# Kernel tuning notes

Hardware: AMD Instinct MI355X
Metric: run time of the kernel (lower is better)

The kernel has to match this reference:

```python
import jax, jax.numpy as jnp
import numpy as np

ALPHA = 0.25
GAMMA = 2.0
# all cost weights are 1.0 per init defaults

def box_cxcywh_to_xyxy(b):
    cx, cy, w, h = b[..., 0], b[..., 1], b[..., 2], b[..., 3]
    return jnp.stack([cx - 0.5 * w, cy - 0.5 * h, cx + 0.5 * w, cy + 0.5 * h], axis=-1)

def generalized_box_iou(b1, b2):
    # b1: [B,Q,4], b2: [B,T,4] in xyxy -> [B,Q,T]
    area1 = (b1[..., 2] - b1[..., 0]) * (b1[..., 3] - b1[..., 1])  # [B,Q]
    area2 = (b2[..., 2] - b2[..., 0]) * (b2[..., 3] - b2[..., 1])  # [B,T]
    lt = jnp.maximum(b1[:, :, None, :2], b2[:, None, :, :2])        # [B,Q,T,2]
    rb = jnp.minimum(b1[:, :, None, 2:], b2[:, None, :, 2:])
    wh = jnp.clip(rb - lt, 0.0)
    inter = wh[..., 0] * wh[..., 1]
    union = area1[:, :, None] + area2[:, None, :] - inter
    iou = inter / union
    lt_c = jnp.minimum(b1[:, :, None, :2], b2[:, None, :, :2])
    rb_c = jnp.maximum(b1[:, :, None, 2:], b2[:, None, :, 2:])
    wh_c = jnp.clip(rb_c - lt_c, 0.0)
    area_c = wh_c[..., 0] * wh_c[..., 1]
    return iou - (area_c - union) / area_c

def point_sample_bilinear(img, pts):
    # img: [B,N,H,W]; pts: [P,2] (x,y) in [0,1]. Matches F.grid_sample
    # bilinear, align_corners=False, padding_mode='zeros'.
    H, W = img.shape[-2], img.shape[-1]
    x = pts[:, 0] * W - 0.5
    y = pts[:, 1] * H - 0.5
    x0 = jnp.floor(x); y0 = jnp.floor(y)
    wx1 = x - x0; wx0 = 1.0 - wx1
    wy1 = y - y0; wy0 = 1.0 - wy1

    def gather(yi, xi):
        valid = ((xi >= 0) & (xi < W) & (yi >= 0) & (yi < H)).astype(img.dtype)
        xc = jnp.clip(xi, 0, W - 1).astype(jnp.int32)
        yc = jnp.clip(yi, 0, H - 1).astype(jnp.int32)
        return img[:, :, yc, xc] * valid  # [B,N,P]

    return (gather(y0, x0) * (wy0 * wx0)
            + gather(y0, x0 + 1) * (wy0 * wx1)
            + gather(y0 + 1, x0) * (wy1 * wx0)
            + gather(y0 + 1, x0 + 1) * (wy1 * wx1))

def point_sample_nearest(img, pts):
    # grid_sample nearest, align_corners=False, zeros padding
    H, W = img.shape[-2], img.shape[-1]
    x = jnp.round(pts[:, 0] * W - 0.5)
    y = jnp.round(pts[:, 1] * H - 0.5)
    valid = ((x >= 0) & (x < W) & (y >= 0) & (y < H)).astype(img.dtype)
    xc = jnp.clip(x, 0, W - 1).astype(jnp.int32)
    yc = jnp.clip(y, 0, H - 1).astype(jnp.int32)
    return img[:, :, yc, xc] * valid  # [B,N,P]

def setup_inputs() -> dict:
    key = jax.random.key(0)
    ks = jax.random.split(key, 7)
    B, Q, C, T, H, W = 2, 900, 91, 64, 128, 128
    P = H * W // 16  # mask_point_sample_ratio = 16
    return {
        "pred_logits": jax.random.normal(ks[0], (B, Q, C), jnp.float32),
        "pred_boxes": jax.random.uniform(ks[1], (B, Q, 4), jnp.float32),
        "pred_masks": jax.random.normal(ks[2], (B, Q, H, W), jnp.float32),
        "tgt_boxes": jax.random.uniform(ks[3], (B, T, 4), jnp.float32),
        "tgt_masks": jax.random.uniform(ks[4], (B, T, H, W), jnp.float32),
        "point_coords": jax.random.uniform(ks[5], (1, P, 2), jnp.float32),
        "tgt_labels": jax.random.randint(ks[6], (B, T), 0, C, jnp.int32),
    }

def reference(pred_logits, pred_boxes, pred_masks, tgt_boxes, tgt_masks, point_coords, tgt_labels):
    # ---- focal classification cost ----
    prob = jax.nn.sigmoid(pred_logits)                          # [B,Q,C]
    neg_cost = (1 - ALPHA) * prob ** GAMMA * (-jax.nn.log_sigmoid(-pred_logits))
    pos_cost = ALPHA * (1 - prob) ** GAMMA * (-jax.nn.log_sigmoid(pred_logits))
    diff = pos_cost - neg_cost                                   # [B,Q,C]
    cost_class = jnp.take_along_axis(diff, tgt_labels[:, None, :], axis=2)  # [B,Q,T]

    # ---- L1 bbox cost (cdist p=1) ----
    cost_bbox = jnp.abs(pred_boxes[:, :, None, :] - tgt_boxes[:, None, :, :]).sum(-1)

    # ---- GIoU cost ----
    giou = generalized_box_iou(box_cxcywh_to_xyxy(pred_boxes), box_cxcywh_to_xyxy(tgt_boxes))

    # ---- point-sampled mask CE / Dice costs ----
    pts = point_coords[0]                                        # [P,2]
    P = pts.shape[0]
    pred_pts = point_sample_bilinear(pred_masks, pts)            # [B,Q,P]
    tgt_pts = point_sample_nearest(tgt_masks, pts)               # [B,T,P]
    pos_ce = -jax.nn.log_sigmoid(pred_pts)
    neg_ce = -jax.nn.log_sigmoid(-pred_pts)
    cost_ce = (jnp.einsum('bqp,btp->bqt', pos_ce, tgt_pts)
               + jnp.einsum('bqp,btp->bqt', neg_ce, 1.0 - tgt_pts)) / P
    s = jax.nn.sigmoid(pred_pts)
    numer = 2.0 * jnp.einsum('bqp,btp->bqt', s, tgt_pts)
    denom = s.sum(-1)[:, :, None] + tgt_pts.sum(-1)[:, None, :]
    cost_dice = 1.0 - (numer + 1.0) / (denom + 1.0)

    C = (cost_bbox + cost_class - giou + cost_ce + cost_dice).astype(jnp.float32)
    # replace non-finite entries by 2 * (per-batch max finite cost)
    fin = jnp.isfinite(C)
    max_cost = jnp.max(jnp.where(fin, C, 0.0), axis=(1, 2), keepdims=True)
    C = jnp.where(fin, C, 2.0 * max_cost)
    return C
```

## Files before the change

kernel.cpp:

```cpp
#include <hip/hip_runtime.h>
#include <hip/hip_bf16.h>
#include <math.h>

#define B_    2
#define Q_    900
#define QPAD_ 912
#define MT_   57
#define CC_   91
#define T_    64
#define H_    128
#define W_    128
#define HW_   (H_*W_)
#define P_    1024
#define FLT_BIG 3.402823466e+38f

typedef short short8 __attribute__((ext_vector_type(8)));
typedef float f32x4  __attribute__((ext_vector_type(4)));

static __device__ __forceinline__ unsigned short f2bf(float v) {
    __hip_bfloat16 h = __float2bfloat16(v);
    return *reinterpret_cast<unsigned short*>(&h);
}

__global__ __launch_bounds__(256) void kS_sample(
    const float* __restrict__ tgt_masks,
    const float* __restrict__ pred_masks,
    const float* __restrict__ pc,
    unsigned short* __restrict__ tgtPT,
    float* __restrict__ tsum,
    unsigned short* __restrict__ xsbuf,
    float* __restrict__ lneg,
    float* __restrict__ lsum,
    float* __restrict__ bmax)
{
    const int tid = threadIdx.x;
    const int wv = tid >> 6, lane = tid & 63;
    __shared__ float sSum[2][4];

    if (blockIdx.x < B_*T_) {
        if (blockIdx.x == 0 && tid < B_) bmax[tid] = 0.f;
        const int bt = blockIdx.x;
        const float* __restrict__ img = tgt_masks + (size_t)bt * HW_;

        float vals[4];
        #pragma unroll
        for (int k = 0; k < 4; ++k) {
            int p = tid*4 + k;
            float px = pc[2*p], py = pc[2*p+1];
            float xf = rintf(px * (float)W_ - 0.5f);
            float yf = rintf(py * (float)H_ - 0.5f);
            bool nv = (xf >= 0.f) && (xf < (float)W_) && (yf >= 0.f) && (yf < (float)H_);
            int xc = (int)fminf(fmaxf(xf, 0.f), (float)(W_-1));
            int yc = (int)fminf(fmaxf(yf, 0.f), (float)(H_-1));
            vals[k] = nv ? img[yc*W_ + xc] : 0.f;
        }
        *(ushort4*)(tgtPT + (size_t)bt*P_ + tid*4) =
            make_ushort4(f2bf(vals[0]), f2bf(vals[1]), f2bf(vals[2]), f2bf(vals[3]));

        float local = (vals[0] + vals[1]) + (vals[2] + vals[3]);
        #pragma unroll
        for (int off = 32; off; off >>= 1) local += __shfl_down(local, off);
        if (lane == 0) sSum[0][wv] = local;
        __syncthreads();
        if (tid == 0) tsum[bt] = (sSum[0][0]+sSum[0][1]) + (sSum[0][2]+sSum[0][3]);
    } else {
        const int bq = blockIdx.x - B_*T_;
        const int b = bq / Q_, q = bq % Q_;
        const float* __restrict__ img = pred_masks + (size_t)bq * HW_;

        int   base0[4], base1[4];
        float wp0[4], wp1[4], wyv0[4], wyv1[4];
        #pragma unroll
        for (int k = 0; k < 4; ++k) {
            int p = tid*4 + k;
            float px = pc[2*p], py = pc[2*p+1];
            float xf = px * (float)W_ - 0.5f;
            float yf = py * (float)H_ - 0.5f;
            float x0f = floorf(xf), y0f = floorf(yf);
            float wx1 = xf - x0f, wx0 = 1.f - wx1;
            float wy1 = yf - y0f, wy0 = 1.f - wy1;
            int x0 = (int)x0f, y0 = (int)y0f;
            int xa = min(max(x0, 0), W_-2);
            wp0[k] = (x0 == xa) ? wx0 : ((x0 < xa) ? wx1 : 0.f);
            wp1[k] = (x0 == xa) ? wx1 : ((x0 > xa) ? wx0 : 0.f);
            wyv0[k] = (y0 >= 0 && y0 < H_)       ? wy0 : 0.f;
            wyv1[k] = (y0+1 >= 0 && y0+1 < H_)   ? wy1 : 0.f;
            int ya0 = min(max(y0,   0), H_-1);
            int ya1 = min(max(y0+1, 0), H_-1);
            base0[k] = ya0*W_ + xa;
            base1[k] = ya1*W_ + xa;
        }

        float2 r0[4], r1[4];
        #pragma unroll
        for (int k = 0; k < 4; ++k) {
            __builtin_memcpy(&r0[k], img + base0[k], 8);
            __builtin_memcpy(&r1[k], img + base1[k], 8);
        }

        float ln = 0.f, ls = 0.f;
        unsigned short px_[4], ps_[4];
        #pragma unroll
        for (int k = 0; k < 4; ++k) {
            float x = wyv0[k]*(wp0[k]*r0[k].x + wp1[k]*r0[k].y)
                    + wyv1[k]*(wp0[k]*r1[k].x + wp1[k]*r1[k].y);
            float e  = __expf(-fabsf(x));
            float sp = __logf(1.f + e) + fmaxf(x, 0.f);
            float rr = 1.f / (1.f + e);
            float s  = (x >= 0.f) ? rr : e * rr;
            ln += sp; ls += s;
            px_[k] = f2bf(x); ps_[k] = f2bf(s);
        }

        *(ushort4*)(xsbuf + ((size_t)(b*2+0)*QPAD_ + q)*P_ + tid*4) = make_ushort4(px_[0],px_[1],px_[2],px_[3]);
        *(ushort4*)(xsbuf + ((size_t)(b*2+1)*QPAD_ + q)*P_ + tid*4) = make_ushort4(ps_[0],ps_[1],ps_[2],ps_[3]);

        #pragma unroll
        for (int off = 32; off; off >>= 1) {
            ln += __shfl_down(ln, off);
            ls += __shfl_down(ls, off);
        }
        if (lane == 0) { sSum[0][wv] = ln; sSum[1][wv] = ls; }
        __syncthreads();
        if (tid == 0) {
            lneg[b*Q_ + q] = (sSum[0][0]+sSum[0][1]) + (sSum[0][2]+sSum[0][3]);
            lsum[b*Q_ + q] = (sSum[1][0]+sSum[1][1]) + (sSum[1][2]+sSum[1][3]);
        }
    }
}

__global__ __launch_bounds__(256) void k3_gemm(
    const unsigned short* __restrict__ xsbuf,
    const unsigned short* __restrict__ tgtPT,
    const float* __restrict__ lneg,
    const float* __restrict__ lsum,
    const float* __restrict__ tsum,
    const float* __restrict__ pred_logits,
    const float* __restrict__ pred_boxes,
    const float* __restrict__ tgt_boxes,
    const int*   __restrict__ tgt_labels,
    float* __restrict__ out,
    float* __restrict__ bmax)
{
    __shared__ float sT[2][4][4][65];

    const int bid = blockIdx.x;
    const int b = bid / (MT_*4);
    const int rem = bid % (MT_*4);
    const int mt = rem >> 2, nt = rem & 3;
    const int w = threadIdx.x >> 6, l = threadIdx.x & 63;
    const int ml = l & 15, kg = l >> 4;

    const short* Ax = (const short*)xsbuf + ((size_t)(b*2+0)*QPAD_ + mt*16 + ml)*P_ + kg*8 + w*256;
    const short* As = (const short*)xsbuf + ((size_t)(b*2+1)*QPAD_ + mt*16 + ml)*P_ + kg*8 + w*256;
    const short* Bb = (const short*)tgtPT + ((size_t)(b*T_) + nt*16 + ml)*P_ + kg*8 + w*256;

    f32x4 accX = {0,0,0,0};
    f32x4 accS = {0,0,0,0};

    #pragma unroll
    for (int kt = 0; kt < 8; ++kt) {
        const int ko = kt * 32;
        short8 afx = *(const short8*)(Ax + ko);
        short8 afs = *(const short8*)(As + ko);
        short8 bf  = *(const short8*)(Bb + ko);
        accX = __builtin_amdgcn_mfma_f32_16x16x32_bf16(afx, bf, accX, 0, 0, 0);
        accS = __builtin_amdgcn_mfma_f32_16x16x32_bf16(afs, bf, accS, 0, 0, 0);
    }

    #pragma unroll
    for (int r = 0; r < 4; ++r) {
        sT[0][r][w][l] = accX[r];
        sT[1][r][w][l] = accS[r];
    }
    __syncthreads();

    const int tid = threadIdx.x;
    const int ql = tid >> 4, tc = tid & 15;
    const int r   = ql & 3;
    const int src = (ql >> 2)*16 + tc;

    float aX = ((sT[0][r][0][src] + sT[0][r][1][src]) + (sT[0][r][2][src] + sT[0][r][3][src]));
    float aS = ((sT[1][r][0][src] + sT[1][r][1][src]) + (sT[1][r][2][src] + sT[1][r][3][src]));

    const int q = mt*16 + ql;
    const int t = nt*16 + tc;
    const int qc = min(q, Q_-1);

    const float tsu = tsum[b*T_ + t];
    const int   lab = tgt_labels[b*T_ + t];
    const float4 tbx = *(const float4*)(tgt_boxes + (size_t)(b*T_ + t)*4);
    float ln  = lneg[b*Q_ + qc];
    float lsv = lsum[b*Q_ + qc];
    float4 pb = *(const float4*)(pred_boxes + (size_t)(b*Q_ + qc)*4);
    float lg  = pred_logits[((size_t)(b*Q_ + qc))*CC_ + lab];

    float ce   = (ln - aX) * (1.f/(float)P_);
    float dice = 1.f - (2.f*aS + 1.f) / (lsv + tsu + 1.f);

    float e  = __expf(-fabsf(lg));
    float lp = log1pf(e);
    float sp_neg = lp + fmaxf(-lg, 0.f);
    float sp_pos = lp + fmaxf( lg, 0.f);
    float prob = 1.f / (1.f + __expf(-lg));
    float cclass = 0.25f*(1.f-prob)*(1.f-prob)*sp_neg - 0.75f*prob*prob*sp_pos;

    float cbbox = fabsf(pb.x-tbx.x) + fabsf(pb.y-tbx.y) + fabsf(pb.z-tbx.z) + fabsf(pb.w-tbx.w);
    float px1 = pb.x - 0.5f*pb.z, py1 = pb.y - 0.5f*pb.w;
    float px2 = pb.x + 0.5f*pb.z, py2 = pb.y + 0.5f*pb.w;
    float tx1 = tbx.x - 0.5f*tbx.z, ty1 = tbx.y - 0.5f*tbx.w;
    float tx2 = tbx.x + 0.5f*tbx.z, ty2 = tbx.y + 0.5f*tbx.w;
    float a1 = (px2-px1)*(py2-py1);
    float a2 = (tx2-tx1)*(ty2-ty1);
    float iw = fmaxf(fminf(px2,tx2) - fmaxf(px1,tx1), 0.f);
    float ih = fmaxf(fminf(py2,ty2) - fmaxf(py1,ty1), 0.f);
    float inter = iw*ih;
    float uni = a1 + a2 - inter;
    float iou = inter / uni;
    float cw = fmaxf(fmaxf(px2,tx2) - fminf(px1,tx1), 0.f);
    float ch = fmaxf(fmaxf(py2,ty2) - fminf(py1,ty1), 0.f);
    float ac = cw*ch;
    float giou = iou - (ac - uni)/ac;

    float cost = cbbox + cclass - giou + ce + dice;
    float mloc = 0.f;
    if (q < Q_) {
        out[((size_t)(b*Q_ + q))*T_ + t] = cost;
        mloc = (fabsf(cost) <= FLT_BIG) ? fmaxf(cost, 0.f) : 0.f;
    }

    #pragma unroll
    for (int off = 32; off; off >>= 1) mloc = fmaxf(mloc, __shfl_down(mloc, off));
    __shared__ float sm[4];
    if (l == 0) sm[w] = mloc;
    __syncthreads();
    if (tid == 0) {
        float bm = fmaxf(fmaxf(sm[0], sm[1]), fmaxf(sm[2], sm[3]));
        atomicMax((unsigned int*)&bmax[b], __float_as_uint(bm));
    }
}

__global__ __launch_bounds__(256) void k5_fix(float* __restrict__ out,
                                              const float* __restrict__ bmax)
{
    int i = blockIdx.x*256 + threadIdx.x;
    if (i >= B_*Q_*T_) return;
    float v = out[i];
    if (!(fabsf(v) <= FLT_BIG))
        out[i] = 2.f * bmax[i / (Q_*T_)];
}

extern "C" void kernel_launch(void* const* d_in, const int* in_sizes, int n_in,
                              void* d_out, int out_size, void* d_ws, size_t ws_size,
                              hipStream_t stream) {
    const float* pred_logits  = (const float*)d_in[0];
    const float* pred_boxes   = (const float*)d_in[1];
    const float* pred_masks   = (const float*)d_in[2];
    const float* tgt_boxes    = (const float*)d_in[3];
    const float* tgt_masks    = (const float*)d_in[4];
    const float* point_coords = (const float*)d_in[5];
    const int*   tgt_labels   = (const int*)d_in[6];
    float* out = (float*)d_out;

    char* w = (char*)d_ws;
    unsigned short* tgtPT = (unsigned short*)w;
    unsigned short* xsbuf = (unsigned short*)(w + 262144);
    size_t xs_bytes = (size_t)B_*2*QPAD_*P_*2;
    char* w2 = w + 262144 + xs_bytes;
    float* tsum = (float*)w2;
    float* lneg = (float*)(w2 + 512);
    float* lsum = (float*)(w2 + 512 + 7296);
    float* bmax = (float*)(w2 + 512 + 2*7296);

    kS_sample<<<B_*T_ + B_*Q_, 256, 0, stream>>>(tgt_masks, pred_masks, point_coords,
                                                 tgtPT, tsum, xsbuf, lneg, lsum, bmax);
    k3_gemm<<<B_*MT_*4, 256, 0, stream>>>(xsbuf, tgtPT, lneg, lsum, tsum,
                                          pred_logits, pred_boxes, tgt_boxes, tgt_labels, out, bmax);
    k5_fix<<<(B_*Q_*T_ + 255)/256, 256, 0, stream>>>(out, bmax);
}
```

Measured before the change: 47.63 us.

## Stage full mask images into LDS via async global_load_lds before point sampling

Each sampling block copies its entire 128x128 mask into shared memory with direct global-to-LDS loads, then performs the nearest and bilinear gathers from LDS. This replaces scattered global gathers with coalesced bulk loads. It uses 64 KB of LDS per block, which limits occupancy, and it reads every pixel even where only sampled pixels are needed.

```diff
diff --git a/kernel.cpp b/kernel.cpp
--- a/kernel.cpp
+++ b/kernel.cpp
@@ -14,6 +14,9 @@
 #define P_    1024
 #define FLT_BIG 3.402823466e+38f
 
+#define AS1 __attribute__((address_space(1)))
+#define AS3 __attribute__((address_space(3)))
+
 typedef short short8 __attribute__((ext_vector_type(8)));
 typedef float f32x4  __attribute__((ext_vector_type(4)));
 
@@ -33,16 +36,32 @@
     float* __restrict__ lsum,
     float* __restrict__ bmax)
 {
+    __shared__ float simg[HW_];
+    __shared__ float sSum[2][4];
+
     const int tid = threadIdx.x;
     const int wv = tid >> 6, lane = tid & 63;
-    __shared__ float sSum[2][4];
-
-    if (blockIdx.x < B_*T_) {
+    const bool isTgt = (blockIdx.x < (B_*T_));
+    const float* __restrict__ img = isTgt
+        ? (tgt_masks  + (size_t)blockIdx.x * HW_)
+        : (pred_masks + (size_t)(blockIdx.x - B_*T_) * HW_);
+
+    {
+        const float* gbase = img  + wv*4096 + lane*4;
+        float*       lbase = simg + wv*4096;
+        #pragma unroll
+        for (int it = 0; it < 16; ++it) {
+            __builtin_amdgcn_global_load_lds((const AS1 float*)(gbase + it*256),
+                                             (AS3 float*)(lbase + it*256),
+                                             16, 0, 0);
+        }
+    }
+
+    if (isTgt) {
         if (blockIdx.x == 0 && tid < B_) bmax[tid] = 0.f;
         const int bt = blockIdx.x;
-        const float* __restrict__ img = tgt_masks + (size_t)bt * HW_;
-
-        float vals[4];
+
+        int   nidx[4];
         #pragma unroll
         for (int k = 0; k < 4; ++k) {
             int p = tid*4 + k;
@@ -52,8 +71,15 @@
             bool nv = (xf >= 0.f) && (xf < (float)W_) && (yf >= 0.f) && (yf < (float)H_);
             int xc = (int)fminf(fmaxf(xf, 0.f), (float)(W_-1));
             int yc = (int)fminf(fmaxf(yf, 0.f), (float)(H_-1));
-            vals[k] = nv ? img[yc*W_ + xc] : 0.f;
-        }
+            nidx[k] = nv ? (yc*W_ + xc) : -1;
+        }
+        __syncthreads();
+
+        float vals[4];
+        #pragma unroll
+        for (int k = 0; k < 4; ++k)
+            vals[k] = (nidx[k] >= 0) ? simg[nidx[k]] : 0.f;
+
         *(ushort4*)(tgtPT + (size_t)bt*P_ + tid*4) =
             make_ushort4(f2bf(vals[0]), f2bf(vals[1]), f2bf(vals[2]), f2bf(vals[3]));
 
@@ -66,44 +92,48 @@
     } else {
         const int bq = blockIdx.x - B_*T_;
         const int b = bq / Q_, q = bq % Q_;
-        const float* __restrict__ img = pred_masks + (size_t)bq * HW_;
-
-        int   base0[4], base1[4];
-        float wp0[4], wp1[4], wyv0[4], wyv1[4];
+
+        int   o[4][4];
+        float ww[4][4];
         #pragma unroll
         for (int k = 0; k < 4; ++k) {
             int p = tid*4 + k;
             float px = pc[2*p], py = pc[2*p+1];
-            float xf = px * (float)W_ - 0.5f;
-            float yf = py * (float)H_ - 0.5f;
-            float x0f = floorf(xf), y0f = floorf(yf);
-            float wx1 = xf - x0f, wx0 = 1.f - wx1;
-            float wy1 = yf - y0f, wy0 = 1.f - wy1;
+            float x = px * (float)W_ - 0.5f;
+            float y = py * (float)H_ - 0.5f;
+            float x0f = floorf(x), y0f = floorf(y);
+            float wx1 = x - x0f, wy1 = y - y0f;
+            float wx0 = 1.f - wx1, wy0 = 1.f - wy1;
             int x0 = (int)x0f, y0 = (int)y0f;
-            int xa = min(max(x0, 0), W_-2);
-            wp0[k] = (x0 == xa) ? wx0 : ((x0 < xa) ? wx1 : 0.f);
-            wp1[k] = (x0 == xa) ? wx1 : ((x0 > xa) ? wx0 : 0.f);
-            wyv0[k] = (y0 >= 0 && y0 < H_)       ? wy0 : 0.f;
-            wyv1[k] = (y0+1 >= 0 && y0+1 < H_)   ? wy1 : 0.f;
-            int ya0 = min(max(y0,   0), H_-1);
-            int ya1 = min(max(y0+1, 0), H_-1);
-            base0[k] = ya0*W_ + xa;
-            base1[k] = ya1*W_ + xa;
-        }
-
-        float2 r0[4], r1[4];
+            int   xs2[2] = {x0, x0+1}, ys2[2] = {y0, y0+1};
+            float wxs[2] = {wx0, wx1}, wys[2] = {wy0, wy1};
+            #pragma unroll
+            for (int dy = 0; dy < 2; ++dy)
+            #pragma unroll
+            for (int dx = 0; dx < 2; ++dx) {
+                int xi = xs2[dx], yi = ys2[dy];
+                bool v = (xi >= 0) && (xi < W_) && (yi >= 0) && (yi < H_);
+                int xcc = min(max(xi, 0), W_-1);
+                int ycc = min(max(yi, 0), H_-1);
+                o [k][dy*2+dx] = ycc*W_ + xcc;
+                ww[k][dy*2+dx] = v ? wys[dy]*wxs[dx] : 0.f;
+            }
+        }
+        __syncthreads();
+
+        float tap[4][4];
         #pragma unroll
         for (int k = 0; k < 4; ++k) {
-            __builtin_memcpy(&r0[k], img + base0[k], 8);
-            __builtin_memcpy(&r1[k], img + base1[k], 8);
+            tap[k][0] = simg[o[k][0]]; tap[k][1] = simg[o[k][1]];
+            tap[k][2] = simg[o[k][2]]; tap[k][3] = simg[o[k][3]];
         }
 
         float ln = 0.f, ls = 0.f;
         unsigned short px_[4], ps_[4];
         #pragma unroll
         for (int k = 0; k < 4; ++k) {
-            float x = wyv0[k]*(wp0[k]*r0[k].x + wp1[k]*r0[k].y)
-                    + wyv1[k]*(wp0[k]*r1[k].x + wp1[k]*r1[k].y);
+            float x = ww[k][0]*tap[k][0] + ww[k][1]*tap[k][1]
+                    + ww[k][2]*tap[k][2] + ww[k][3]*tap[k][3];
             float e  = __expf(-fabsf(x));
             float sp = __logf(1.f + e) + fmaxf(x, 0.f);
             float rr = 1.f / (1.f + e);
```

Result: faster. 39.38 us (median of 2 runs) (-17.3%).
